# Kernel optimization log

Hardware: AMD Instinct MI355X
Metric: run time of the kernel (lower is better)

Reference implementation:

```python
import jax, jax.numpy as jnp
import numpy as np

NF = 16            # num_frequencies
S = 2              # scale_factor
MAX_STD = 0.5
POS_LIMIT = 1.0


def setup_inputs() -> dict:
    key = jax.random.key(0)
    ks = jax.random.split(key, 8)
    B, G, H, W = 16, 256, 128, 128
    hidden, base = 1024, 256
    in_dim = (G + 2 * NF + 1) * S * S  # 4624
    # xavier-uniform-like scales
    lim1 = float(np.sqrt(6.0 / (hidden + in_dim)))
    lim2 = float(np.sqrt(6.0 / (base + hidden)))
    return {
        "position": jax.random.uniform(ks[0], (B, 4), dtype=jnp.float32),
        "gestalt": jax.random.normal(ks[1], (B, G), dtype=jnp.float32),
        "mask": jax.random.uniform(ks[2], (B, 1, H, W), dtype=jnp.float32),
        "depth": jax.random.normal(ks[3], (B, 1, H, W), dtype=jnp.float32),
        "weight1": jax.random.uniform(ks[4], (hidden, in_dim), minval=-lim1, maxval=lim1, dtype=jnp.float32),
        "bias1": jnp.zeros((hidden,), dtype=jnp.float32),
        "weight2": jax.random.uniform(ks[5], (base, hidden), minval=-lim2, maxval=lim2, dtype=jnp.float32),
        "bias2": jnp.zeros((base,), dtype=jnp.float32),
    }


def reference(position, gestalt, mask, depth, weight1, bias1, weight2, bias2):
    B, _, H, W = mask.shape
    # positional grids in [-1, 1], shapes (1,1,H,W)
    gx = (jnp.arange(W, dtype=jnp.float32) / (W - 1)) * 2 - 1
    gy = (jnp.arange(H, dtype=jnp.float32) / (H - 1)) * 2 - 1
    grid_y, grid_x = jnp.meshgrid(gy, gx, indexing="ij")
    grid_x = grid_x[None, None]
    grid_y = grid_y[None, None]

    x = jnp.clip(position[:, 0], -POS_LIMIT, POS_LIMIT)[:, None, None, None]
    y = jnp.clip(position[:, 1], -POS_LIMIT, POS_LIMIT)[:, None, None, None]
    min_std = 1.0 / min(H, W)
    std = 0.1 / jnp.clip(position[:, 3], min_std, MAX_STD)[:, None, None, None]
    std_y = std
    std_x = std * (W / H)

    half_pi = jnp.float32(np.pi / 2)
    ngx = (grid_x - x) * std_x * half_pi  # (B,1,H,W)
    ngy = (grid_y - y) * std_y * half_pi
    freqs = (2.0 ** jnp.arange(NF, dtype=jnp.float32))[None, :, None, None]
    cos_x = jnp.cos(ngx * freqs)  # (B,NF,H,W)
    cos_y = jnp.cos(ngy * freqs)
    # interleave: [cx0, cy0, cx1, cy1, ...]
    embedding = jnp.stack([cos_x, cos_y], axis=2).reshape(B, 2 * NF, H, W)

    inp = jnp.concatenate(
        [gestalt[:, :, None, None] * mask, embedding * mask, depth * mask], axis=1
    )  # (B,C,H,W)
    C = inp.shape[1]
    # space-to-depth patchify
    p = inp.reshape(B, C, H // S, S, W // S, S)
    p = p.transpose(0, 2, 4, 1, 3, 5).reshape(B * (H // S) * (W // S), C * S * S)

    h = p @ weight1.T + bias1
    h = h * jax.nn.sigmoid(h)  # SiLU
    o = h @ weight2.T + bias2
    return o.reshape(B, H // S, W // S, -1).transpose(0, 3, 1, 2)
```

## Files before the change

kernel.cpp:

```cpp
#include <hip/hip_runtime.h>
#include <cstdio>


#define NFREQ 16
#define BB 16
#define G 256
#define KIN 1156
#define K1 144
#define STAGE_U16 12800

typedef unsigned short u16;
using bf16x8 = __bf16 __attribute__((ext_vector_type(8)));
using f32x16 = float __attribute__((ext_vector_type(16)));
using f32x4  = float __attribute__((ext_vector_type(4)));

__device__ __forceinline__ u16 f2bf(float f) {
  unsigned u = __float_as_uint(f);
  u += 0x7fffu + ((u >> 16) & 1u);
  return (u16)(u >> 16);
}
__device__ __forceinline__ unsigned pk2(float a, float b) {
  return (unsigned)f2bf(a) | ((unsigned)f2bf(b) << 16);
}
__device__ __forceinline__ unsigned pk2f(float a, float b) {
  unsigned ua = __float_as_uint(a) + 0x8000u;
  unsigned ub = __float_as_uint(b) + 0x8000u;
  return __builtin_amdgcn_perm(ub, ua, 0x07060302u);
}
__device__ __forceinline__ float silu(float h) {
  float e = __builtin_amdgcn_exp2f(h * -1.44269504088896f);
  return h * __builtin_amdgcn_rcpf(1.f + e);
}
__device__ __forceinline__ void gl_lds16(const u16* g, u16* l) {
  __builtin_amdgcn_global_load_lds(
      (const __attribute__((address_space(1))) void*)g,
      (__attribute__((address_space(3))) void*)l, 16, 0, 0);
}

__global__ void k_pre(const float* __restrict__ pos,
                      const float* __restrict__ gestalt,
                      const float* __restrict__ w1,
                      const float* __restrict__ w2,
                      const float* __restrict__ bias1,
                      float* __restrict__ cosx, float* __restrict__ cosy,
                      u16* __restrict__ B1F, u16* __restrict__ W2F) {
  const int bid = blockIdx.x;
  const int t = threadIdx.x;

  if (bid < 1024) {
    __shared__ float w1row[KIN];
    __shared__ float gestT[G * BB];
    __shared__ float psum[256];
    __shared__ float wg[64];
    const int n = bid;
    const float b1v = bias1[n];
    for (int i = t; i < KIN; i += 256) w1row[i] = w1[(size_t)n * KIN + i];
    for (int i = t; i < BB * G; i += 256) {
      int bb = i >> 8, c = i & 255;
      gestT[c * BB + bb] = gestalt[i];
    }
    __syncthreads();
    {
      int bb = t & 15, j = (t >> 4) & 3, q = t >> 6;
      float acc = 0.f;
#pragma unroll 8
      for (int c = q * 64; c < q * 64 + 64; ++c)
        acc += gestT[c * BB + bb] * w1row[4 * c + j];
      psum[t] = acc;
    }
    __syncthreads();
    if (t < 64) {
      int bb = t >> 2, j = t & 3;
      wg[t] = psum[j * 16 + bb] + psum[64 + j * 16 + bb] +
              psum[128 + j * 16 + bb] + psum[192 + j * 16 + bb];
    }
    __syncthreads();
    const int ch = n >> 5, l31n = n & 31;
    for (int c = t; c < BB * (K1 / 8); c += 256) {
      int bb = c / 18, kc = c - bb * 18;
      int k0 = kc * 8;
      float v[8];
#pragma unroll
      for (int i = 0; i < 8; ++i) {
        int k = k0 + i;
        float vv;
        if (k < 64)       vv = w1row[1024 + 8 * (k >> 2) + (k & 3)];
        else if (k < 128) { int kk = k - 64; vv = w1row[1024 + 8 * (kk >> 2) + 4 + (kk & 3)]; }
        else if (k < 132) vv = wg[bb * 4 + (k - 128)];
        else if (k < 136) vv = w1row[1152 + (k - 132)];
        else if (k == 136) vv = b1v;
        else              vv = 0.f;
        v[i] = vv;
      }
      uint4 u;
      u.x = pk2(v[0], v[1]); u.y = pk2(v[2], v[3]);
      u.z = pk2(v[4], v[5]); u.w = pk2(v[6], v[7]);
      size_t idx0 = ((((size_t)bb * 32 + ch) * 9 + (kc >> 1)) * 64 +
                     (kc & 1) * 32 + l31n) * 8;
      *(uint4*)(B1F + idx0) = u;
    }
  } else if (bid < 1152) {
    int e8 = (bid - 1024) * 256 + t;
    int lane = e8 & 63;
    int ct   = (e8 >> 6) & 7;
    int kc   = e8 >> 9;
    int n2 = ct * 32 + (lane & 31);
    int k2 = kc * 16 + (lane >> 5) * 8;
    const float* src = w2 + (size_t)n2 * 1024 + k2;
    uint4 u;
    u.x = pk2(src[0], src[1]); u.y = pk2(src[2], src[3]);
    u.z = pk2(src[4], src[5]); u.w = pk2(src[6], src[7]);
    *(uint4*)(W2F + (size_t)e8 * 8) = u;
  } else {
    int idx = (bid - 1152) * 256 + t;
    int table = idx >> 15;
    int rem = idx & 32767;
    int b = rem >> 11;
    int f = (rem >> 7) & 15;
    int c = rem & 127;
    float p0 = pos[b * 4 + 0];
    float p1 = pos[b * 4 + 1];
    float p3 = pos[b * 4 + 3];
    float x = fminf(fmaxf(p0, -1.f), 1.f);
    float y = fminf(fmaxf(p1, -1.f), 1.f);
    float stdv = 0.1f / fminf(fmaxf(p3, 0.0078125f), 0.5f);
    const float half_pi = 1.57079632679489661923f;
    float g = ((float)c / 127.0f) * 2.0f - 1.0f;
    float ng = (table == 0) ? ((g - x) * stdv) * half_pi
                            : ((g - y) * stdv) * half_pi;
    float freq = (float)(1 << f);
    float val = cosf(ng * freq);
    if (table == 0) cosx[(b * NFREQ + f) * 128 + c] = val;
    else            cosy[(b * NFREQ + f) * 128 + c] = val;
  }
}

__global__ __launch_bounds__(256, 2) void k_main(
    const u16* __restrict__ B1F, const u16* __restrict__ W2F,
    const float* __restrict__ mask, const float* __restrict__ depth,
    const float* __restrict__ cosx, const float* __restrict__ cosy,
    const float* __restrict__ bias2, float* __restrict__ out)
{
  __shared__ __align__(16) u16 sbuf[2 * STAGE_U16];
  float* stg = (float*)sbuf;

  const int tid = threadIdx.x;
  const int w = tid >> 6;
  const int lane = tid & 63;
  const int l31 = lane & 31;
  const int lhi = lane >> 5;
  const int r0 = blockIdx.x * 128;
  const int b = r0 >> 12;
  const int oy0 = (r0 >> 6) & 63;

  {
    const float4* cx4 = (const float4*)(cosx + (size_t)b * 2048);
    ((float4*)stg)[tid]       = cx4[tid];
    ((float4*)stg)[tid + 256] = cx4[tid + 256];
    if (tid < 64)
      stg[2048 + tid] = cosy[((size_t)b * 16 + (tid >> 2)) * 128 + 2 * oy0 + (tid & 3)];
    if (tid < 128) {
      ((float4*)(stg + 2112))[tid] = ((const float4*)(mask  + ((size_t)b * 128 + 2 * oy0) * 128))[tid];
      ((float4*)(stg + 2624))[tid] = ((const float4*)(depth + ((size_t)b * 128 + 2 * oy0) * 128))[tid];
    }
  }
  __syncthreads();

  bf16x8 bfr[9];
  {
    const int r = w * 32 + l31;
    const int oyl = r >> 6, ox = r & 63;
    float m[4], dd[4];
#pragma unroll
    for (int j = 0; j < 4; ++j) {
      int sy = j >> 1, sx = j & 1;
      float mv = stg[2112 + (2 * oyl + sy) * 128 + 2 * ox + sx];
      m[j] = mv;
      dd[j] = stg[2624 + (2 * oyl + sy) * 128 + 2 * ox + sx] * mv;
    }
#pragma unroll
    for (int ks = 0; ks < 9; ++ks) {
      const int k0 = ks * 16 + lhi * 8;
      unsigned dwords[4];
#pragma unroll
      for (int h = 0; h < 4; ++h) {
        float v[2];
#pragma unroll
        for (int p = 0; p < 2; ++p) {
          const int k = k0 + 2 * h + p;
          float vv;
          if (k < 64) {
            const int f = k >> 2, j = k & 3;
            vv = m[j] * stg[f * 128 + 2 * ox + (j & 1)];
          } else if (k < 128) {
            const int kk = k - 64, f = kk >> 2, j = kk & 3;
            vv = m[j] * stg[2048 + f * 4 + 2 * oyl + (j >> 1)];
          } else if (k < 132) {
            vv = m[k - 128];
          } else if (k < 136) {
            vv = dd[k - 132];
          } else if (k == 136) {
            vv = 1.0f;
          } else {
            vv = 0.f;
          }
          v[p] = vv;
        }
        dwords[h] = pk2(v[0], v[1]);
      }
      uint4 u; u.x = dwords[0]; u.y = dwords[1]; u.z = dwords[2]; u.w = dwords[3];
      bfr[ks] = __builtin_bit_cast(bf16x8, u);
    }
  }
  __syncthreads();

  f32x16 acc2[8];
#pragma unroll
  for (int c = 0; c < 8; ++c)
#pragma unroll
    for (int i = 0; i < 16; ++i) acc2[c][i] = 0.f;

  const int naf = (w == 0) ? 3 : 2;
  const int wf0 = 9 + ((w + 3) & 3);
  const u16* b1base = B1F + (size_t)b * 32 * 4608 + lane * 8;
  const u16* w2base = W2F + lane * 8;

  auto prefetch = [&](const u16* asrc, const u16* wsrc, u16* dst) {
#pragma unroll
    for (int j = 0; j < 3; ++j)
      if (j < naf) gl_lds16(asrc + (w + 4 * j) * 512, dst + (w + 4 * j) * 512);
#pragma unroll
    for (int j = 0; j < 4; ++j) {
      const int c = wf0 + 4 * j;
      gl_lds16(wsrc + (c - 9) * 512, dst + c * 512);
    }
  };

  prefetch(b1base, w2base, sbuf);
  __syncthreads();

  for (int ch = 0; ch < 32; ++ch) {
    const int st = ch & 1;
    if (ch + 1 < 32)
      prefetch(b1base + (size_t)(ch + 1) * 4608, w2base + (size_t)(ch + 1) * 8192,
               sbuf + (st ^ 1) * STAGE_U16);

    const u16* afb = sbuf + st * STAGE_U16;
    const u16* wfb = afb + 4608;

    f32x16 acc1;
#pragma unroll
    for (int i = 0; i < 16; ++i) acc1[i] = 0.f;
#pragma unroll
    for (int ks = 0; ks < 9; ++ks) {
      bf16x8 af = *(const bf16x8*)(afb + ks * 512 + lane * 8);
      acc1 = __builtin_amdgcn_mfma_f32_32x32x16_bf16(af, bfr[ks], acc1, 0, 0, 0);
    }

    unsigned d[8];
#pragma unroll
    for (int q = 0; q < 4; ++q) {
      d[2 * q]     = pk2f(silu(acc1[4 * q + 0]), silu(acc1[4 * q + 1]));
      d[2 * q + 1] = pk2f(silu(acc1[4 * q + 2]), silu(acc1[4 * q + 3]));
    }
    unsigned y0 = (unsigned)__shfl_xor((int)(lhi ? d[0] : d[2]), 32);
    unsigned y1 = (unsigned)__shfl_xor((int)(lhi ? d[1] : d[3]), 32);
    unsigned y2 = (unsigned)__shfl_xor((int)(lhi ? d[4] : d[6]), 32);
    unsigned y3 = (unsigned)__shfl_xor((int)(lhi ? d[5] : d[7]), 32);
    uint4 fa, fb;
    fa.x = lhi ? y0 : d[0];  fa.y = lhi ? y1 : d[1];
    fa.z = lhi ? d[2] : y0;  fa.w = lhi ? d[3] : y1;
    fb.x = lhi ? y2 : d[4];  fb.y = lhi ? y3 : d[5];
    fb.z = lhi ? d[6] : y2;  fb.w = lhi ? d[7] : y3;
    bf16x8 fragA = __builtin_bit_cast(bf16x8, fa);
    bf16x8 fragB = __builtin_bit_cast(bf16x8, fb);

#pragma unroll
    for (int ct = 0; ct < 8; ++ct) {
      bf16x8 wf = *(const bf16x8*)(wfb + ct * 512 + lane * 8);
      acc2[ct] = __builtin_amdgcn_mfma_f32_32x32x16_bf16(fragA, wf, acc2[ct], 0, 0, 0);
    }
#pragma unroll
    for (int ct = 0; ct < 8; ++ct) {
      bf16x8 wf = *(const bf16x8*)(wfb + 4096 + ct * 512 + lane * 8);
      acc2[ct] = __builtin_amdgcn_mfma_f32_32x32x16_bf16(fragB, wf, acc2[ct], 0, 0, 0);
    }

    __syncthreads();
  }

#pragma unroll
  for (int ct = 0; ct < 8; ++ct) {
    const int n2 = ct * 32 + l31;
    const float b2 = bias2[n2];
    float* ob = out + ((size_t)b * 256 + n2) * 4096;
#pragma unroll
    for (int q = 0; q < 4; ++q) {
      const int rl = w * 32 + 8 * q + 4 * lhi;
      const int oy = oy0 + (rl >> 6);
      const int ox = rl & 63;
      f32x4 v;
      v[0] = acc2[ct][4 * q + 0] + b2;
      v[1] = acc2[ct][4 * q + 1] + b2;
      v[2] = acc2[ct][4 * q + 2] + b2;
      v[3] = acc2[ct][4 * q + 3] + b2;
      *(f32x4*)(ob + oy * 64 + ox) = v;
    }
  }
}


extern "C" void kernel_launch(void* const* d_in, const int* in_sizes, int n_in,
                              void* d_out, int out_size, void* d_ws, size_t ws_size,
                              hipStream_t stream) {
  const float* pos     = (const float*)d_in[0];
  const float* gestalt = (const float*)d_in[1];
  const float* mask    = (const float*)d_in[2];
  const float* depth   = (const float*)d_in[3];
  const float* w1      = (const float*)d_in[4];
  const float* bias1   = (const float*)d_in[5];
  const float* w2      = (const float*)d_in[6];
  const float* bias2   = (const float*)d_in[7];
  float* out = (float*)d_out;

  const size_t NEED = 131072u + 131072u + 4718592u + 524288u;
  if (ws_size < NEED) {
    fprintf(stderr, "[kernel] ws_size=%zu < needed %zu — skipping launches\n",
            ws_size, NEED);
    return;
  }
  char* ws = (char*)d_ws;
  float* cosx = (float*)(ws);
  float* cosy = (float*)(ws + 131072);
  u16*   B1F  = (u16*)(ws + 262144);
  u16*   W2F  = (u16*)(ws + 262144 + 4718592);

  k_pre<<<1408, 256, 0, stream>>>(pos, gestalt, w1, w2, bias1, cosx, cosy, B1F, W2F);
  k_main<<<512, 256, 0, stream>>>(B1F, W2F, mask, depth, cosx, cosy, bias2, out);
}
```

Measured before the change: 163.8 us.

## Triple-buffer main-loop prefetch, split MFMA chains, use permlane32 swap, pad LDS

The main kernel moves from a double-buffered to a triple-buffered LDS pipeline, issuing prefetches two chunks ahead. It replaces the per-iteration __syncthreads with a manual vmcnt wait plus one barrier. The first GEMM's 9-MFMA dependent chain is split into two accumulators to expose independent MFMAs. The shfl_xor exchange is replaced with v_permlane32_swap, blocks are remapped via a swizzle, and the preprocessing kernel pads its shared transpose buffer to avoid bank conflicts. The trade-off is more LDS per block, which could reduce occupancy, and the hand-tuned vmcnt value depends on the exact number of outstanding loads.

```diff
diff --git a/kernel.cpp b/kernel.cpp
--- a/kernel.cpp
+++ b/kernel.cpp
@@ -8,6 +8,7 @@
 #define KIN 1156
 #define K1 144
 #define STAGE_U16 12800
+#define NSTAGE 3
 
 typedef unsigned short u16;
 using bf16x8 = __bf16 __attribute__((ext_vector_type(8)));
@@ -49,15 +50,17 @@
 
   if (bid < 1024) {
     __shared__ float w1row[KIN];
-    __shared__ float gestT[G * BB];
+    __shared__ float gestT[G * 17];
     __shared__ float psum[256];
     __shared__ float wg[64];
     const int n = bid;
     const float b1v = bias1[n];
+#pragma unroll
     for (int i = t; i < KIN; i += 256) w1row[i] = w1[(size_t)n * KIN + i];
+#pragma unroll
     for (int i = t; i < BB * G; i += 256) {
       int bb = i >> 8, c = i & 255;
-      gestT[c * BB + bb] = gestalt[i];
+      gestT[c * 17 + bb] = gestalt[i];
     }
     __syncthreads();
     {
@@ -65,7 +68,7 @@
       float acc = 0.f;
 #pragma unroll 8
       for (int c = q * 64; c < q * 64 + 64; ++c)
-        acc += gestT[c * BB + bb] * w1row[4 * c + j];
+        acc += gestT[c * 17 + bb] * w1row[4 * c + j];
       psum[t] = acc;
     }
     __syncthreads();
@@ -141,7 +144,7 @@
     const float* __restrict__ cosx, const float* __restrict__ cosy,
     const float* __restrict__ bias2, float* __restrict__ out)
 {
-  __shared__ __align__(16) u16 sbuf[2 * STAGE_U16];
+  __shared__ __align__(16) u16 sbuf[NSTAGE * STAGE_U16];
   float* stg = (float*)sbuf;
 
   const int tid = threadIdx.x;
@@ -149,7 +152,8 @@
   const int lane = tid & 63;
   const int l31 = lane & 31;
   const int lhi = lane >> 5;
-  const int r0 = blockIdx.x * 128;
+  const int bswz = (blockIdx.x & 7) * 64 + (blockIdx.x >> 3);
+  const int r0 = bswz * 128;
   const int b = r0 >> 12;
   const int oy0 = (r0 >> 6) & 63;
 
@@ -225,7 +229,9 @@
   const u16* b1base = B1F + (size_t)b * 32 * 4608 + lane * 8;
   const u16* w2base = W2F + lane * 8;
 
-  auto prefetch = [&](const u16* asrc, const u16* wsrc, u16* dst) {
+  auto prefetch = [&](int ch, u16* dst) {
+    const u16* asrc = b1base + (size_t)ch * 4608;
+    const u16* wsrc = w2base + (size_t)ch * 8192;
 #pragma unroll
     for (int j = 0; j < 3; ++j)
       if (j < naf) gl_lds16(asrc + (w + 4 * j) * 512, dst + (w + 4 * j) * 512);
@@ -236,44 +242,63 @@
     }
   };
 
-  prefetch(b1base, w2base, sbuf);
-  __syncthreads();
-
+  prefetch(0, sbuf);
+  prefetch(1, sbuf + STAGE_U16);
+
+  int st = 0;
   for (int ch = 0; ch < 32; ++ch) {
-    const int st = ch & 1;
-    if (ch + 1 < 32)
-      prefetch(b1base + (size_t)(ch + 1) * 4608, w2base + (size_t)(ch + 1) * 8192,
-               sbuf + (st ^ 1) * STAGE_U16);
+    if (ch < 31) asm volatile("s_waitcnt vmcnt(6)" ::: "memory");
+    else         asm volatile("s_waitcnt vmcnt(0)" ::: "memory");
+    __builtin_amdgcn_s_barrier();
+    asm volatile("" ::: "memory");
+    __builtin_amdgcn_sched_barrier(0);
+
+    if (ch + 2 < 32) {
+      int s2 = st + 2; if (s2 >= NSTAGE) s2 -= NSTAGE;
+      prefetch(ch + 2, sbuf + s2 * STAGE_U16);
+    }
 
     const u16* afb = sbuf + st * STAGE_U16;
     const u16* wfb = afb + 4608;
 
-    f32x16 acc1;
-#pragma unroll
-    for (int i = 0; i < 16; ++i) acc1[i] = 0.f;
-#pragma unroll
-    for (int ks = 0; ks < 9; ++ks) {
-      bf16x8 af = *(const bf16x8*)(afb + ks * 512 + lane * 8);
-      acc1 = __builtin_amdgcn_mfma_f32_32x32x16_bf16(af, bfr[ks], acc1, 0, 0, 0);
+    f32x16 a1a, a1b;
+#pragma unroll
+    for (int i = 0; i < 16; ++i) { a1a[i] = 0.f; a1b[i] = 0.f; }
+#pragma unroll
+    for (int ks = 0; ks < 4; ++ks) {
+      bf16x8 af0 = *(const bf16x8*)(afb + (2 * ks) * 512 + lane * 8);
+      bf16x8 af1 = *(const bf16x8*)(afb + (2 * ks + 1) * 512 + lane * 8);
+      a1a = __builtin_amdgcn_mfma_f32_32x32x16_bf16(af0, bfr[2 * ks],     a1a, 0, 0, 0);
+      a1b = __builtin_amdgcn_mfma_f32_32x32x16_bf16(af1, bfr[2 * ks + 1], a1b, 0, 0, 0);
+    }
+    {
+      bf16x8 af8 = *(const bf16x8*)(afb + 8 * 512 + lane * 8);
+      a1a = __builtin_amdgcn_mfma_f32_32x32x16_bf16(af8, bfr[8], a1a, 0, 0, 0);
     }
 
     unsigned d[8];
 #pragma unroll
     for (int q = 0; q < 4; ++q) {
-      d[2 * q]     = pk2f(silu(acc1[4 * q + 0]), silu(acc1[4 * q + 1]));
-      d[2 * q + 1] = pk2f(silu(acc1[4 * q + 2]), silu(acc1[4 * q + 3]));
-    }
-    unsigned y0 = (unsigned)__shfl_xor((int)(lhi ? d[0] : d[2]), 32);
-    unsigned y1 = (unsigned)__shfl_xor((int)(lhi ? d[1] : d[3]), 32);
-    unsigned y2 = (unsigned)__shfl_xor((int)(lhi ? d[4] : d[6]), 32);
-    unsigned y3 = (unsigned)__shfl_xor((int)(lhi ? d[5] : d[7]), 32);
-    uint4 fa, fb;
-    fa.x = lhi ? y0 : d[0];  fa.y = lhi ? y1 : d[1];
-    fa.z = lhi ? d[2] : y0;  fa.w = lhi ? d[3] : y1;
-    fb.x = lhi ? y2 : d[4];  fb.y = lhi ? y3 : d[5];
-    fb.z = lhi ? d[6] : y2;  fb.w = lhi ? d[7] : y3;
-    bf16x8 fragA = __builtin_bit_cast(bf16x8, fa);
-    bf16x8 fragB = __builtin_bit_cast(bf16x8, fb);
+      float s0 = silu(a1a[4 * q + 0] + a1b[4 * q + 0]);
+      float s1 = silu(a1a[4 * q + 1] + a1b[4 * q + 1]);
+      float s2 = silu(a1a[4 * q + 2] + a1b[4 * q + 2]);
+      float s3 = silu(a1a[4 * q + 3] + a1b[4 * q + 3]);
+      d[2 * q]     = pk2f(s0, s1);
+      d[2 * q + 1] = pk2f(s2, s3);
+    }
+    unsigned e0 = d[0], e1 = d[2];
+    unsigned e2 = d[1], e3 = d[3];
+    unsigned e4 = d[4], e5 = d[6];
+    unsigned e6 = d[5], e7 = d[7];
+    asm("v_permlane32_swap_b32 %0, %1" : "+v"(e0), "+v"(e1));
+    asm("v_permlane32_swap_b32 %0, %1" : "+v"(e2), "+v"(e3));
+    asm("v_permlane32_swap_b32 %0, %1" : "+v"(e4), "+v"(e5));
+    asm("v_permlane32_swap_b32 %0, %1" : "+v"(e6), "+v"(e7));
+    uint4 fav, fbv;
+    fav.x = e0; fav.y = e2; fav.z = e1; fav.w = e3;
+    fbv.x = e4; fbv.y = e6; fbv.z = e5; fbv.w = e7;
+    bf16x8 fragA = __builtin_bit_cast(bf16x8, fav);
+    bf16x8 fragB = __builtin_bit_cast(bf16x8, fbv);
 
 #pragma unroll
     for (int ct = 0; ct < 8; ++ct) {
@@ -286,7 +311,7 @@
       acc2[ct] = __builtin_amdgcn_mfma_f32_32x32x16_bf16(fragB, wf, acc2[ct], 0, 0, 0);
     }
 
-    __syncthreads();
+    if (++st == NSTAGE) st = 0;
   }
 
 #pragma unroll
```

New measurement: 157.9 us. -3.6%, faster.
